# Kernel tuning notes

Measured on AMD Instinct MI355X. Metric: run time of the kernel, lower is better.

Reference implementation:

```python
import jax, jax.numpy as jnp
import numpy as np

B = 64      # 'batch' init arg: projected-away input dim
N = 8192    # sequence length after transpose
DK = 64     # dk, used only for 1/sqrt(dk) scaling


def setup_inputs() -> dict:
    key = jax.random.key(0)
    ks = jax.random.split(key, 9)
    f32 = jnp.float32
    q = jax.random.normal(ks[0], (B, N), f32)
    k = jax.random.normal(ks[1], (B, N), f32)
    v = jax.random.normal(ks[2], (B, N), f32)
    # Linear(B -> 1) params, torch-style: weight [1, B], bias [1]
    s = 1.0 / np.sqrt(B)
    Wq = jax.random.uniform(ks[3], (1, B), f32, -s, s)
    bq = jax.random.uniform(ks[4], (1,), f32, -s, s)
    Wk = jax.random.uniform(ks[5], (1, B), f32, -s, s)
    bk = jax.random.uniform(ks[6], (1,), f32, -s, s)
    Wv = jax.random.uniform(ks[7], (1, B), f32, -s, s)
    bv = jax.random.uniform(ks[8], (1,), f32, -s, s)
    return {"q": q, "k": k, "v": v, "Wq": Wq, "bq": bq,
            "Wk": Wk, "bk": bk, "Wv": Wv, "bv": bv}


def reference(q, k, v, Wq, bq, Wk, bk, Wv, bv):
    # q,k,v: [B, N]; transpose(0,1) then Linear(B -> 1) => [N, 1]
    qp = q.T @ Wq.T + bq          # [N, 1]
    kp = k.T @ Wk.T + bk          # [N, 1]
    vp = v.T @ Wv.T + bv          # [N, 1]
    scale = 1.0 / jnp.sqrt(jnp.asarray(DK, q.dtype))
    scores = (qp @ kp.T) * scale  # [N, N] rank-1 outer product
    attn = jax.nn.softmax(scores, axis=-1)  # [N, N]
    out = attn @ vp               # [N, 1]
    return (out, attn)
```

## Files before the change

### kernel.cpp

```cpp
#include <hip/hip_runtime.h>

#define N 8192

using f4 = __attribute__((ext_vector_type(4))) float;

__global__ __launch_bounds__(256) void proj_kernel(
    const float* __restrict__ q, const float* __restrict__ k, const float* __restrict__ v,
    const float* __restrict__ Wq, const float* __restrict__ bq,
    const float* __restrict__ Wk, const float* __restrict__ bk,
    const float* __restrict__ Wv, const float* __restrict__ bv,
    float* __restrict__ aq, float* __restrict__ kp, float* __restrict__ vp)
{
    const int tn = threadIdx.x & 63;
    const int tb = threadIdx.x >> 6;
    const int n  = blockIdx.x * 64 + tn;
    float sq = 0.f, sk = 0.f, sv = 0.f;
#pragma unroll
    for (int bi = 0; bi < 16; ++bi) {
        const int b = tb * 16 + bi;
        sq = fmaf(q[b * N + n], Wq[b], sq);
        sk = fmaf(k[b * N + n], Wk[b], sk);
        sv = fmaf(v[b * N + n], Wv[b], sv);
    }
    __shared__ float red[3][4][64];
    red[0][tb][tn] = sq; red[1][tb][tn] = sk; red[2][tb][tn] = sv;
    __syncthreads();
    if (tb == 0) {
        const float fq = red[0][0][tn] + red[0][1][tn] + red[0][2][tn] + red[0][3][tn];
        const float fk = red[1][0][tn] + red[1][1][tn] + red[1][2][tn] + red[1][3][tn];
        const float fv = red[2][0][tn] + red[2][1][tn] + red[2][2][tn] + red[2][3][tn];
        aq[n] = (fq + bq[0]) * 0.125f;
        kp[n] = fk + bk[0];
        vp[n] = fv + bv[0];
    }
}

__global__ __launch_bounds__(512) void attn_kernel(
    const float* __restrict__ aq, const float* __restrict__ kp, const float* __restrict__ vp,
    float* __restrict__ out, float* __restrict__ attn)
{
    __shared__ float kl[N];
    __shared__ float vl[N];
    __shared__ float wmax[8], wmin[8];
    const int tid  = threadIdx.x;
    const int lane = tid & 63;
    const int wave = tid >> 6;

    float lmax = -1e30f, lmin = 1e30f;
#pragma unroll
    for (int it = 0; it < 4; ++it) {
        const int i4 = tid + it * 512;
        const f4 kk = reinterpret_cast<const f4*>(kp)[i4];
        const f4 vv = reinterpret_cast<const f4*>(vp)[i4];
        reinterpret_cast<f4*>(kl)[i4] = kk;
        reinterpret_cast<f4*>(vl)[i4] = vv;
        lmax = fmaxf(lmax, fmaxf(fmaxf(kk[0], kk[1]), fmaxf(kk[2], kk[3])));
        lmin = fminf(lmin, fminf(fminf(kk[0], kk[1]), fminf(kk[2], kk[3])));
    }
#pragma unroll
    for (int off = 32; off; off >>= 1) {
        lmax = fmaxf(lmax, __shfl_xor(lmax, off));
        lmin = fminf(lmin, __shfl_xor(lmin, off));
    }
    if (lane == 0) { wmax[wave] = lmax; wmin[wave] = lmin; }
    __syncthreads();
    float kmax = wmax[0], kmin = wmin[0];
#pragma unroll
    for (int w = 1; w < 8; ++w) { kmax = fmaxf(kmax, wmax[w]); kmin = fminf(kmin, wmin[w]); }

    for (int rr = 0; rr < 2; ++rr) {
        const int r = blockIdx.x * 16 + wave * 2 + rr;
        const float a = aq[r];
        const float m = (a >= 0.f) ? a * kmax : a * kmin;
        float s = 0.f, o = 0.f;
#pragma unroll 8
        for (int it = 0; it < 32; ++it) {
            const f4 kk = reinterpret_cast<const f4*>(kl)[lane + it * 64];
            const f4 vv = reinterpret_cast<const f4*>(vl)[lane + it * 64];
            const float e0 = __expf(fmaf(a, kk[0], -m));
            const float e1 = __expf(fmaf(a, kk[1], -m));
            const float e2 = __expf(fmaf(a, kk[2], -m));
            const float e3 = __expf(fmaf(a, kk[3], -m));
            s += (e0 + e1) + (e2 + e3);
            o = fmaf(e0, vv[0], o);
            o = fmaf(e1, vv[1], o);
            o = fmaf(e2, vv[2], o);
            o = fmaf(e3, vv[3], o);
        }
#pragma unroll
        for (int off = 32; off; off >>= 1) {
            s += __shfl_xor(s, off);
            o += __shfl_xor(o, off);
        }
        const float inv = 1.0f / s;
        if (lane == 0) out[r] = o * inv;

        f4* __restrict__ arow = reinterpret_cast<f4*>(attn + (size_t)r * N);
#pragma unroll 8
        for (int it = 0; it < 32; ++it) {
            const f4 kk = reinterpret_cast<const f4*>(kl)[lane + it * 64];
            f4 e;
            e[0] = __expf(fmaf(a, kk[0], -m)) * inv;
            e[1] = __expf(fmaf(a, kk[1], -m)) * inv;
            e[2] = __expf(fmaf(a, kk[2], -m)) * inv;
            e[3] = __expf(fmaf(a, kk[3], -m)) * inv;
            __builtin_nontemporal_store(e, &arow[lane + it * 64]);
        }
    }
}

extern "C" void kernel_launch(void* const* d_in, const int* in_sizes, int n_in,
                              void* d_out, int out_size, void* d_ws, size_t ws_size,
                              hipStream_t stream)
{
    const float* q  = (const float*)d_in[0];
    const float* k  = (const float*)d_in[1];
    const float* v  = (const float*)d_in[2];
    const float* Wq = (const float*)d_in[3];
    const float* bq = (const float*)d_in[4];
    const float* Wk = (const float*)d_in[5];
    const float* bk = (const float*)d_in[6];
    const float* Wv = (const float*)d_in[7];
    const float* bv = (const float*)d_in[8];

    float* out  = (float*)d_out;
    float* attn = out + N;

    float* aq = (float*)d_ws;
    float* kp = aq + N;
    float* vp = kp + N;

    proj_kernel<<<128, 256, 0, stream>>>(q, k, v, Wq, bq, Wk, bk, Wv, bv, aq, kp, vp);
    attn_kernel<<<512, 512, 0, stream>>>(aq, kp, vp, out, attn);
}
```

Baseline: 62.45 us.

## Cache exponentials in registers, use native exp2, and halve attn grid

```diff
diff --git a/kernel.cpp b/kernel.cpp
--- a/kernel.cpp
+++ b/kernel.cpp
@@ -1,8 +1,15 @@
 #include <hip/hip_runtime.h>
 
 #define N 8192
+#define LOG2E 1.4426950408889634f
 
 using f4 = __attribute__((ext_vector_type(4))) float;
+
+#if __has_builtin(__builtin_amdgcn_exp2f)
+#define EXP2(x) __builtin_amdgcn_exp2f(x)
+#else
+#define EXP2(x) exp2f(x)
+#endif
 
 __global__ __launch_bounds__(256) void proj_kernel(
     const float* __restrict__ q, const float* __restrict__ k, const float* __restrict__ v,
@@ -29,13 +36,13 @@
         const float fq = red[0][0][tn] + red[0][1][tn] + red[0][2][tn] + red[0][3][tn];
         const float fk = red[1][0][tn] + red[1][1][tn] + red[1][2][tn] + red[1][3][tn];
         const float fv = red[2][0][tn] + red[2][1][tn] + red[2][2][tn] + red[2][3][tn];
-        aq[n] = (fq + bq[0]) * 0.125f;
+        aq[n] = (fq + bq[0]) * 0.125f * LOG2E;
         kp[n] = fk + bk[0];
         vp[n] = fv + bv[0];
     }
 }
 
-__global__ __launch_bounds__(512) void attn_kernel(
+__global__ __launch_bounds__(512, 2) void attn_kernel(
     const float* __restrict__ aq, const float* __restrict__ kp, const float* __restrict__ vp,
     float* __restrict__ out, float* __restrict__ attn)
 {
@@ -68,24 +75,29 @@
 #pragma unroll
     for (int w = 1; w < 8; ++w) { kmax = fmaxf(kmax, wmax[w]); kmin = fminf(kmin, wmin[w]); }
 
-    for (int rr = 0; rr < 2; ++rr) {
-        const int r = blockIdx.x * 16 + wave * 2 + rr;
-        const float a = aq[r];
-        const float m = (a >= 0.f) ? a * kmax : a * kmin;
+    for (int rr = 0; rr < 4; ++rr) {
+        const int r = blockIdx.x * 32 + wave * 4 + rr;
+        const float a2 = aq[r];
+        const float m2 = (a2 >= 0.f) ? a2 * kmax : a2 * kmin;
+        const float nm2 = -m2;
+
+        f4 e[32];
         float s = 0.f, o = 0.f;
-#pragma unroll 8
+#pragma unroll
         for (int it = 0; it < 32; ++it) {
             const f4 kk = reinterpret_cast<const f4*>(kl)[lane + it * 64];
             const f4 vv = reinterpret_cast<const f4*>(vl)[lane + it * 64];
-            const float e0 = __expf(fmaf(a, kk[0], -m));
-            const float e1 = __expf(fmaf(a, kk[1], -m));
-            const float e2 = __expf(fmaf(a, kk[2], -m));
-            const float e3 = __expf(fmaf(a, kk[3], -m));
-            s += (e0 + e1) + (e2 + e3);
-            o = fmaf(e0, vv[0], o);
-            o = fmaf(e1, vv[1], o);
-            o = fmaf(e2, vv[2], o);
-            o = fmaf(e3, vv[3], o);
+            f4 ee;
+            ee[0] = EXP2(fmaf(a2, kk[0], nm2));
+            ee[1] = EXP2(fmaf(a2, kk[1], nm2));
+            ee[2] = EXP2(fmaf(a2, kk[2], nm2));
+            ee[3] = EXP2(fmaf(a2, kk[3], nm2));
+            s += (ee[0] + ee[1]) + (ee[2] + ee[3]);
+            o = fmaf(ee[0], vv[0], o);
+            o = fmaf(ee[1], vv[1], o);
+            o = fmaf(ee[2], vv[2], o);
+            o = fmaf(ee[3], vv[3], o);
+            e[it] = ee;
         }
 #pragma unroll
         for (int off = 32; off; off >>= 1) {
@@ -96,15 +108,11 @@
         if (lane == 0) out[r] = o * inv;
 
         f4* __restrict__ arow = reinterpret_cast<f4*>(attn + (size_t)r * N);
-#pragma unroll 8
+#pragma unroll
         for (int it = 0; it < 32; ++it) {
-            const f4 kk = reinterpret_cast<const f4*>(kl)[lane + it * 64];
-            f4 e;
-            e[0] = __expf(fmaf(a, kk[0], -m)) * inv;
-            e[1] = __expf(fmaf(a, kk[1], -m)) * inv;
-            e[2] = __expf(fmaf(a, kk[2], -m)) * inv;
-            e[3] = __expf(fmaf(a, kk[3], -m)) * inv;
-            __builtin_nontemporal_store(e, &arow[lane + it * 64]);
+            f4 w = e[it];
+            w[0] *= inv; w[1] *= inv; w[2] *= inv; w[3] *= inv;
+            __builtin_nontemporal_store(w, &arow[lane + it * 64]);
         }
     }
 }
@@ -131,5 +139,5 @@
     float* vp = kp + N;
 
     proj_kernel<<<128, 256, 0, stream>>>(q, k, v, Wq, bq, Wk, bk, Wv, bv, aq, kp, vp);
-    attn_kernel<<<512, 512, 0, stream>>>(aq, kp, vp, out, attn);
+    attn_kernel<<<256, 512, 0, stream>>>(aq, kp, vp, out, attn);
 }
```

After: 113.7 us. +82.1%, slower.
